# Optimization experiments

Measured on AMD Instinct MI355X. Metric: run time of the kernel, lower is better.

The kernel has to match this reference:

```python
import jax, jax.numpy as jnp
import numpy as np

EPS = 1e-3  # Keras BatchNormalization default epsilon


def _bn(x, gamma, beta, mean, var):
    # inference-mode batchnorm over channel axis 1 of [N,C,T,V]
    s = (gamma * jax.lax.rsqrt(var + EPS)).reshape(1, -1, 1, 1)
    b = (beta - gamma * mean * jax.lax.rsqrt(var + EPS)).reshape(1, -1, 1, 1)
    return x * s + b


def setup_inputs() -> dict:
    key = jax.random.key(0)
    ks = jax.random.split(key, 10)
    N, C, T, V, K, F, KT = 64, 64, 300, 25, 3, 64, 9
    x = jax.random.normal(ks[0], (N, C, T, V), jnp.float32)
    W1 = jax.random.normal(ks[1], (C, F * K), jnp.float32) * 0.05
    b1 = jnp.zeros((F * K,), jnp.float32)
    A = jax.random.normal(ks[2], (K, T, V, V), jnp.float32) * 0.2
    gamma1 = jnp.ones((F,), jnp.float32)
    beta1 = jnp.zeros((F,), jnp.float32)
    mean1 = jax.random.normal(ks[3], (F,), jnp.float32) * 0.1
    var1 = jax.random.uniform(ks[4], (F,), jnp.float32) + 0.5
    Wt = jax.random.normal(ks[5], (KT, 1, F, F), jnp.float32) * 0.05  # HWIO
    bt = jnp.zeros((F,), jnp.float32)
    gamma2 = jnp.ones((F,), jnp.float32)
    beta2 = jnp.zeros((F,), jnp.float32)
    mean2 = jax.random.normal(ks[6], (F,), jnp.float32) * 0.1
    var2 = jax.random.uniform(ks[7], (F,), jnp.float32) + 0.5
    return dict(x=x, W1=W1, b1=b1, A=A, gamma1=gamma1, beta1=beta1,
                mean1=mean1, var1=var1, Wt=Wt, bt=bt, gamma2=gamma2,
                beta2=beta2, mean2=mean2, var2=var2)


def reference(x, W1, b1, A, gamma1, beta1, mean1, var1, Wt, bt,
              gamma2, beta2, mean2, var2):
    N, C, T, V = x.shape
    K = A.shape[0]
    F = W1.shape[1] // K
    # SGTACN: 1x1 conv (channels_first) == channel matmul
    y = jnp.einsum('nctv,cf->nftv', x, W1) + b1.reshape(1, -1, 1, 1)
    y = y.reshape(N, K, F, T, V)
    # spatial graph contraction with learned per-timestep adjacency
    y = jnp.einsum('nkftv,ktvw->nftw', y, A)
    # tgcn: BN -> relu -> temporal conv [9,1] SAME -> BN
    y = jax.nn.relu(_bn(y, gamma1, beta1, mean1, var1))
    y = jax.lax.conv_general_dilated(
        y, Wt, window_strides=(1, 1), padding='SAME',
        dimension_numbers=('NCHW', 'HWIO', 'NCHW')) + bt.reshape(1, -1, 1, 1)
    y = _bn(y, gamma2, beta2, mean2, var2)
    # identity residual (stride=1, no downsample, C_in == filters) + relu
    return jax.nn.relu(y + x)
```

## Files before the change

kernel.cpp:

```cpp
#include <hip/hip_runtime.h>
#include <hip/hip_bf16.h>
#include <stdint.h>

#define EPS 1e-3f

typedef __attribute__((ext_vector_type(8))) short bf16x8;
typedef __attribute__((ext_vector_type(4))) float f32x4;

union B8U { bf16x8 v; uint32_t u[4]; };

__device__ inline uint32_t pk2(float a, float b) {
    __hip_bfloat162 p;
    p.x = __float2bfloat16(a);
    p.y = __float2bfloat16(b);
    return *(uint32_t*)&p;
}

__global__ __launch_bounds__(256) void k0_prep_small(
    const float* __restrict__ W1, const float* __restrict__ Wt,
    const float* __restrict__ A,
    uint16_t* __restrict__ W1t, uint16_t* __restrict__ Abf,
    float* __restrict__ csA_g)
{
    int i = blockIdx.x * 256 + threadIdx.x;
    if (i < 12288) {
        int f = i / 192, Kp = i % 192, k = Kp >> 6, c = Kp & 63;
        __hip_bfloat16 b = __float2bfloat16(W1[c * 192 + k * 64 + f]);
        W1t[i] = *(uint16_t*)&b;
    } else if (i < 49152) {
        int j = i - 12288;
        int jj = j & 7, fo = (j >> 3) & 63, kb = j >> 9;
        int kk = kb * 8 + jj, dt = kk >> 6, fi = kk & 63;
        __hip_bfloat16 b = __float2bfloat16(Wt[(dt * 64 + fi) * 64 + fo]);
        Abf[j] = *(uint16_t*)&b;
    } else if (i < 71652) {
        int j = i - 49152;
        int k = j / 7500, r = j % 7500;
        int t = r / 25, w = r % 25;
        float s = 0.f;
        for (int v = 0; v < 25; ++v)
            s += A[((k * 300 + t) * 25 + v) * 25 + w];
        csA_g[j] = s;
    }
}

__global__ __launch_bounds__(256) void k0_prep_At(
    const float* __restrict__ A, uint16_t* __restrict__ At_g)
{
    int i = blockIdx.x * 256 + threadIdx.x;
    if (i < 921600) {
        int v = i & 31, w = (i >> 5) & 31, rest = i >> 10;
        int t = rest % 300, k = rest / 300;
        float val = 0.f;
        if (v < 25 && w < 25)
            val = A[((k * 300 + t) * 25 + v) * 25 + w];
        __hip_bfloat16 b = __float2bfloat16(val);
        At_g[i] = *(uint16_t*)&b;
    }
}

#define K1_SMEM 80512
__global__ __launch_bounds__(256) void k1_fused(
    const float* __restrict__ x, const uint16_t* __restrict__ At_g,
    const uint16_t* __restrict__ W1t, const float* __restrict__ csA_g,
    const float* __restrict__ b1,
    const float* __restrict__ gamma1, const float* __restrict__ beta1,
    const float* __restrict__ mean1, const float* __restrict__ var1,
    uint32_t* __restrict__ h2u)
{
    extern __shared__ __align__(16) char smem[];
    float* csA_s = (float*)(smem + 76800);
    float* s1s   = (float*)(smem + 79200);
    float* b1ns  = (float*)(smem + 79456);
    float* b1s   = (float*)(smem + 79712);

    const int t0   = blockIdx.x * 8;
    const int n    = blockIdx.y;
    const int tid  = threadIdx.x;
    const int lane = tid & 63, wv = tid >> 6;
    const int l15  = lane & 15, g = lane >> 4;
    int vc = (300 - t0) * 25; if (vc > 200) vc = 200;
    const int validcols = vc;

    for (int i = tid; i < 600; i += 256) {
        int k = i / 200, cr = i % 200;
        csA_s[k * 200 + cr] = (cr < validcols) ? csA_g[k * 7500 + t0 * 25 + cr] : 0.f;
    }
    if (tid < 64) {
        float rs = rsqrtf(var1[tid] + EPS);
        s1s[tid]  = gamma1[tid] * rs;
        b1ns[tid] = beta1[tid] - gamma1[tid] * mean1[tid] * rs;
    }
    if (tid >= 64 && tid < 256) b1s[tid - 64] = b1[tid - 64];

    for (int ti = 0; ti < 2; ++ti) {
        const int trel = wv * 2 + ti;
        const int t = t0 + trel;
        if (t >= 300) continue;

        bf16x8 a[4];
        const float* xb = x + (size_t)n * 480000 + t * 25;
        #pragma unroll
        for (int mf = 0; mf < 4; ++mf) {
            const int c = l15 + mf * 16;
            const float* xr = xb + (size_t)c * 7500;
            B8U ua;
            if (g < 3) {
                #pragma unroll
                for (int p = 0; p < 4; ++p)
                    ua.u[p] = pk2(xr[g * 8 + 2 * p], xr[g * 8 + 2 * p + 1]);
            } else {
                ua.u[0] = pk2(xr[24], 0.f);
                ua.u[1] = 0; ua.u[2] = 0; ua.u[3] = 0;
            }
            a[mf] = ua.v;
        }

        f32x4 acc[4][6];
        #pragma unroll
        for (int mf = 0; mf < 4; ++mf)
            #pragma unroll
            for (int nf = 0; nf < 6; ++nf)
                acc[mf][nf] = (f32x4){0.f, 0.f, 0.f, 0.f};

        #pragma unroll
        for (int nf = 0; nf < 6; ++nf) {
            const int col = nf * 16 + l15;
            const int k = col >> 5, w = col & 31;
            bf16x8 b = *(const bf16x8*)(At_g + (((k * 300 + t) * 32 + w) * 32 + g * 8));
            acc[0][nf] = __builtin_amdgcn_mfma_f32_16x16x32_bf16(a[0], b, acc[0][nf], 0, 0, 0);
            acc[1][nf] = __builtin_amdgcn_mfma_f32_16x16x32_bf16(a[1], b, acc[1][nf], 0, 0, 0);
            acc[2][nf] = __builtin_amdgcn_mfma_f32_16x16x32_bf16(a[2], b, acc[2][nf], 0, 0, 0);
            acc[3][nf] = __builtin_amdgcn_mfma_f32_16x16x32_bf16(a[3], b, acc[3][nf], 0, 0, 0);
        }

        #pragma unroll
        for (int nf = 0; nf < 6; ++nf) {
            const int col = nf * 16 + l15;
            const int k = col >> 5, w = col & 31;
            if (w < 25) {
                const int colrow = trel * 25 + w;
                const int sw = (w & 7) << 4;
                #pragma unroll
                for (int mf = 0; mf < 4; ++mf) {
                    const int c0 = mf * 16 + g * 4;
                    const int off = colrow * 384 + (((k * 64 + c0) * 2) ^ sw);
                    uint2 val;
                    val.x = pk2(acc[mf][nf][0], acc[mf][nf][1]);
                    val.y = pk2(acc[mf][nf][2], acc[mf][nf][3]);
                    *(uint2*)(smem + off) = val;
                }
            }
        }
    }
    __syncthreads();

    const int nfbase = (wv == 0) ? 0 : 1 + 3 * wv;
    const int nfcnt  = (wv == 0) ? 4 : 3;

    int coladdr[4], swz[4], colv[4];
    #pragma unroll
    for (int q = 0; q < 4; ++q) {
        int col = (nfbase + q) * 16 + l15;
        colv[q] = col;
        coladdr[q] = col * 384;
        swz[q] = ((col % 25) & 7) << 4;
    }

    f32x4 accz[4][4];
    #pragma unroll
    for (int mf = 0; mf < 4; ++mf)
        #pragma unroll
        for (int q = 0; q < 4; ++q)
            accz[mf][q] = (f32x4){0.f, 0.f, 0.f, 0.f};

    for (int kb = 0; kb < 6; ++kb) {
        bf16x8 a[4];
        #pragma unroll
        for (int mf = 0; mf < 4; ++mf) {
            int f = l15 + mf * 16;
            a[mf] = *(const bf16x8*)(W1t + f * 192 + kb * 32 + g * 8);
        }
        #pragma unroll
        for (int q = 0; q < 4; ++q) {
            if (q < nfcnt) {
                bf16x8 b = *(const bf16x8*)(smem + coladdr[q] + ((kb * 64 + g * 16) ^ swz[q]));
                accz[0][q] = __builtin_amdgcn_mfma_f32_16x16x32_bf16(a[0], b, accz[0][q], 0, 0, 0);
                accz[1][q] = __builtin_amdgcn_mfma_f32_16x16x32_bf16(a[1], b, accz[1][q], 0, 0, 0);
                accz[2][q] = __builtin_amdgcn_mfma_f32_16x16x32_bf16(a[2], b, accz[2][q], 0, 0, 0);
                accz[3][q] = __builtin_amdgcn_mfma_f32_16x16x32_bf16(a[3], b, accz[3][q], 0, 0, 0);
            }
        }
    }

    const uint32_t hbase = (uint32_t)(n * 300 + t0) * 800;
    #pragma unroll
    for (int q = 0; q < 4; ++q) {
        if (q < nfcnt) {
            const int col = colv[q];
            if (col < validcols) {
                const int trel = col / 25, w = col - trel * 25;
                const float cs0 = csA_s[col];
                const float cs1 = csA_s[200 + col];
                const float cs2 = csA_s[400 + col];
                const uint32_t rowbase = hbase + trel * 800 + w * 32;
                #pragma unroll
                for (int mf = 0; mf < 4; ++mf) {
                    const int f0 = mf * 16 + g * 4;
                    float zz[4];
                    #pragma unroll
                    for (int r = 0; r < 4; ++r) {
                        const int f = f0 + r;
                        float z = accz[mf][q][r]
                                + b1s[f] * cs0 + b1s[64 + f] * cs1 + b1s[128 + f] * cs2;
                        z = z * s1s[f] + b1ns[f];
                        zz[r] = fmaxf(z, 0.f);
                    }
                    uint2 st;
                    st.x = pk2(zz[0], zz[1]);
                    st.y = pk2(zz[2], zz[3]);
                    *(uint2*)(h2u + rowbase + (f0 >> 1)) = st;
                }
            }
        }
    }
}

#define K2_SMEM 77312
__global__ __launch_bounds__(256) void k2_mfma(
    const char* __restrict__ h2b,
    const uint16_t* __restrict__ Abf,
    const float* __restrict__ bt,
    const float* __restrict__ gamma2, const float* __restrict__ beta2,
    const float* __restrict__ mean2,  const float* __restrict__ var2,
    const float* __restrict__ x,
    float* __restrict__ out)
{
    extern __shared__ __align__(16) char smem2[];
    char*  lds_h = smem2;
    float* s2s   = (float*)(smem2 + 76800);
    float* b2s   = s2s + 64;

    const int t0  = blockIdx.x * 16;
    const int n   = blockIdx.y;
    const int tid = threadIdx.x;

    if (tid < 64) {
        float rs = rsqrtf(var2[tid] + EPS);
        float s  = gamma2[tid] * rs;
        s2s[tid] = s;
        b2s[tid] = beta2[tid] - gamma2[tid] * mean2[tid] * rs + bt[tid] * s;
    }

    const size_t hn = (size_t)n * 300 * 3200;
    for (int c = tid; c < 4800; c += 256) {
        int rr = c >> 3, c8 = c & 7;
        int trow = rr / 25;
        int w = rr - trow * 25;
        int tg = t0 - 4 + trow;
        int4 v = make_int4(0, 0, 0, 0);
        if (tg >= 0 && tg < 300)
            v = *(const int4*)(h2b + hn + (size_t)tg * 3200 + w * 128 + (c8 << 4));
        int s = c << 4;
        *(int4*)(lds_h + (s ^ (((s >> 7) & 7) << 4))) = v;
    }
    __syncthreads();

    const int wv = tid >> 6, lane = tid & 63;
    const int l15 = lane & 15, g = lane >> 4;
    const int colbase = wv * 112;
    const int nfr = (wv == 3) ? 4 : 7;

    f32x4 acc[4][7];
    #pragma unroll
    for (int mf = 0; mf < 4; ++mf)
        #pragma unroll
        for (int nf = 0; nf < 7; ++nf)
            acc[mf][nf] = (f32x4){0.f, 0.f, 0.f, 0.f};

    for (int kk = 0; kk < 18; ++kk) {
        const int dt   = kk >> 1;
        const int half = (kk & 1) << 6;
        const int kb   = kk * 4 + g;
        bf16x8 a[4];
        #pragma unroll
        for (int mf = 0; mf < 4; ++mf)
            a[mf] = *(const bf16x8*)(Abf + (kb * 64 + l15 + mf * 16) * 8);
        #pragma unroll
        for (int nf = 0; nf < 7; ++nf) {
            if (nf < nfr) {
                int r = colbase + (nf << 4) + l15 + 25 * dt;
                int s = (r << 7) + half + (g << 4);
                bf16x8 b = *(const bf16x8*)(lds_h + (s ^ ((r & 7) << 4)));
                acc[0][nf] = __builtin_amdgcn_mfma_f32_16x16x32_bf16(a[0], b, acc[0][nf], 0, 0, 0);
                acc[1][nf] = __builtin_amdgcn_mfma_f32_16x16x32_bf16(a[1], b, acc[1][nf], 0, 0, 0);
                acc[2][nf] = __builtin_amdgcn_mfma_f32_16x16x32_bf16(a[2], b, acc[2][nf], 0, 0, 0);
                acc[3][nf] = __builtin_amdgcn_mfma_f32_16x16x32_bf16(a[3], b, acc[3][nf], 0, 0, 0);
            }
        }
    }

    const size_t outn = (size_t)n * 480000;
    #pragma unroll
    for (int mf = 0; mf < 4; ++mf) {
        #pragma unroll
        for (int nf = 0; nf < 7; ++nf) {
            if (nf < nfr) {
                int col  = colbase + (nf << 4) + l15;
                int gcol = t0 * 25 + col;
                if (gcol < 7500) {
                    #pragma unroll
                    for (int reg = 0; reg < 4; ++reg) {
                        int fo = (mf << 4) + (g << 2) + reg;
                        size_t ga = outn + (size_t)fo * 7500 + gcol;
                        float val = acc[mf][nf][reg] * s2s[fo] + b2s[fo];
                        out[ga] = fmaxf(val + x[ga], 0.f);
                    }
                }
            }
        }
    }
}

extern "C" void kernel_launch(void* const* d_in, const int* in_sizes, int n_in,
                              void* d_out, int out_size, void* d_ws, size_t ws_size,
                              hipStream_t stream) {
    const float* x      = (const float*)d_in[0];
    const float* W1     = (const float*)d_in[1];
    const float* b1     = (const float*)d_in[2];
    const float* A      = (const float*)d_in[3];
    const float* gamma1 = (const float*)d_in[4];
    const float* beta1  = (const float*)d_in[5];
    const float* mean1  = (const float*)d_in[6];
    const float* var1   = (const float*)d_in[7];
    const float* Wt     = (const float*)d_in[8];
    const float* bt     = (const float*)d_in[9];
    const float* gamma2 = (const float*)d_in[10];
    const float* beta2  = (const float*)d_in[11];
    const float* mean2  = (const float*)d_in[12];
    const float* var2   = (const float*)d_in[13];
    float* out = (float*)d_out;

    char* ws = (char*)d_ws;
    uint32_t* h2u   = (uint32_t*)ws;
    char*     h2b   = ws;
    uint16_t* At_g  = (uint16_t*)(ws + 61440000);
    uint16_t* W1t   = (uint16_t*)(ws + 63283200);
    uint16_t* Abf   = (uint16_t*)(ws + 63307776);
    float*    csA_g = (float*)   (ws + 63381504);

    hipFuncSetAttribute((const void*)k1_fused,
                        hipFuncAttributeMaxDynamicSharedMemorySize, K1_SMEM);
    hipFuncSetAttribute((const void*)k2_mfma,
                        hipFuncAttributeMaxDynamicSharedMemorySize, K2_SMEM);

    k0_prep_small<<<280, 256, 0, stream>>>(W1, Wt, A, W1t, Abf, csA_g);
    k0_prep_At<<<3600, 256, 0, stream>>>(A, At_g);
    k1_fused<<<dim3(38, 64), 256, K1_SMEM, stream>>>(
        x, At_g, W1t, csA_g, b1, gamma1, beta1, mean1, var1, h2u);
    k2_mfma<<<dim3(19, 64), 256, K2_SMEM, stream>>>(
        h2b, Abf, bt, gamma2, beta2, mean2, var2, x, out);
}
```

Before: 452.5 us.

## Stage x tile cooperatively in LDS and halve k1 time tile to four steps

k1 now processes 4 timesteps per block instead of 8, one per wave, doubling the grid and cutting LDS use so more blocks fit per CU. The x tile is loaded cooperatively by all threads with coalesced-ish reads, converted to bf16 and stored into swizzled LDS, then read back as MFMA fragments, replacing strided per-lane global gathers. Adjacency fragments are prefetched into registers before the staging. The tail handling disappears because 300 is divisible by 4, at the cost of an extra barrier and more redundant setup per block.

```diff
diff --git a/kernel.cpp b/kernel.cpp
--- a/kernel.cpp
+++ b/kernel.cpp
@@ -6,8 +6,6 @@
 
 typedef __attribute__((ext_vector_type(8))) short bf16x8;
 typedef __attribute__((ext_vector_type(4))) float f32x4;
-
-union B8U { bf16x8 v; uint32_t u[4]; };
 
 __device__ inline uint32_t pk2(float a, float b) {
     __hip_bfloat162 p;
@@ -59,7 +57,8 @@
     }
 }
 
-#define K1_SMEM 80512
+#define K1_SMEM 61872
+#define XBASE 43008
 __global__ __launch_bounds__(256) void k1_fused(
     const float* __restrict__ x, const uint16_t* __restrict__ At_g,
     const uint16_t* __restrict__ W1t, const float* __restrict__ csA_g,
@@ -69,22 +68,46 @@
     uint32_t* __restrict__ h2u)
 {
     extern __shared__ __align__(16) char smem[];
-    float* csA_s = (float*)(smem + 76800);
-    float* s1s   = (float*)(smem + 79200);
-    float* b1ns  = (float*)(smem + 79456);
-    float* b1s   = (float*)(smem + 79712);
-
-    const int t0   = blockIdx.x * 8;
+    float* csA_s = (float*)(smem + 59392);
+    float* s1s   = (float*)(smem + 60592);
+    float* b1ns  = (float*)(smem + 60848);
+    float* b1s   = (float*)(smem + 61104);
+
+    const int t0   = blockIdx.x * 4;
     const int n    = blockIdx.y;
     const int tid  = threadIdx.x;
     const int lane = tid & 63, wv = tid >> 6;
     const int l15  = lane & 15, g = lane >> 4;
-    int vc = (300 - t0) * 25; if (vc > 200) vc = 200;
-    const int validcols = vc;
-
-    for (int i = tid; i < 600; i += 256) {
-        int k = i / 200, cr = i % 200;
-        csA_s[k * 200 + cr] = (cr < validcols) ? csA_g[k * 7500 + t0 * 25 + cr] : 0.f;
+
+    const int tw = t0 + wv;
+    bf16x8 bfr[6];
+    #pragma unroll
+    for (int nf = 0; nf < 6; ++nf) {
+        const int col = nf * 16 + l15;
+        const int k = col >> 5, w = col & 31;
+        bfr[nf] = *(const bf16x8*)(At_g + (((k * 300 + tw) * 32 + w) * 32 + g * 8));
+    }
+
+    const float* xn = x + (size_t)n * 480000;
+    for (int it = tid; it < 3328; it += 256) {
+        const int c = it / 52;
+        const int r = it % 52;
+        const int trel = r / 13, vp = r % 13;
+        const int v = vp * 2;
+        const float* p = xn + c * 7500 + (t0 + trel) * 25 + v;
+        const int slot = XBASE + (((((v >> 3) * 64 + c) * 4 + trel) * 16) ^ ((c & 7) << 4));
+        if (vp < 12) {
+            *(uint32_t*)(smem + slot + ((v & 7) << 1)) = pk2(p[0], p[1]);
+        } else {
+            *(uint32_t*)(smem + slot + 0)  = pk2(p[0], 0.f);
+            *(uint32_t*)(smem + slot + 4)  = 0u;
+            *(uint32_t*)(smem + slot + 8)  = 0u;
+            *(uint32_t*)(smem + slot + 12) = 0u;
+        }
+    }
+    for (int i = tid; i < 300; i += 256) {
+        int k = i / 100, cr = i % 100;
+        csA_s[i] = csA_g[k * 7500 + t0 * 25 + cr];
     }
     if (tid < 64) {
         float rs = rsqrtf(var1[tid] + EPS);
@@ -92,129 +115,107 @@
         b1ns[tid] = beta1[tid] - gamma1[tid] * mean1[tid] * rs;
     }
     if (tid >= 64 && tid < 256) b1s[tid - 64] = b1[tid - 64];
-
-    for (int ti = 0; ti < 2; ++ti) {
-        const int trel = wv * 2 + ti;
-        const int t = t0 + trel;
-        if (t >= 300) continue;
-
-        bf16x8 a[4];
-        const float* xb = x + (size_t)n * 480000 + t * 25;
-        #pragma unroll
-        for (int mf = 0; mf < 4; ++mf) {
-            const int c = l15 + mf * 16;
-            const float* xr = xb + (size_t)c * 7500;
-            B8U ua;
-            if (g < 3) {
-                #pragma unroll
-                for (int p = 0; p < 4; ++p)
-                    ua.u[p] = pk2(xr[g * 8 + 2 * p], xr[g * 8 + 2 * p + 1]);
-            } else {
-                ua.u[0] = pk2(xr[24], 0.f);
-                ua.u[1] = 0; ua.u[2] = 0; ua.u[3] = 0;
-            }
-            a[mf] = ua.v;
-        }
-
-        f32x4 acc[4][6];
-        #pragma unroll
-        for (int mf = 0; mf < 4; ++mf)
+    __syncthreads();
+
+    bf16x8 a[4];
+    #pragma unroll
+    for (int mf = 0; mf < 4; ++mf) {
+        const int c = l15 + 16 * mf;
+        const int sb = XBASE + ((((g * 64 + c) * 4 + wv) * 16) ^ ((c & 7) << 4));
+        a[mf] = *(const bf16x8*)(smem + sb);
+    }
+
+    f32x4 acc[4][6];
+    #pragma unroll
+    for (int mf = 0; mf < 4; ++mf)
+        #pragma unroll
+        for (int nf = 0; nf < 6; ++nf)
+            acc[mf][nf] = (f32x4){0.f, 0.f, 0.f, 0.f};
+
+    #pragma unroll
+    for (int nf = 0; nf < 6; ++nf) {
+        acc[0][nf] = __builtin_amdgcn_mfma_f32_16x16x32_bf16(a[0], bfr[nf], acc[0][nf], 0, 0, 0);
+        acc[1][nf] = __builtin_amdgcn_mfma_f32_16x16x32_bf16(a[1], bfr[nf], acc[1][nf], 0, 0, 0);
+        acc[2][nf] = __builtin_amdgcn_mfma_f32_16x16x32_bf16(a[2], bfr[nf], acc[2][nf], 0, 0, 0);
+        acc[3][nf] = __builtin_amdgcn_mfma_f32_16x16x32_bf16(a[3], bfr[nf], acc[3][nf], 0, 0, 0);
+    }
+
+    #pragma unroll
+    for (int nf = 0; nf < 6; ++nf) {
+        const int col = nf * 16 + l15;
+        const int k = col >> 5, w = col & 31;
+        if (w < 25) {
+            const int colrow = wv * 25 + w;
+            const int sw = (w & 7) << 4;
             #pragma unroll
-            for (int nf = 0; nf < 6; ++nf)
-                acc[mf][nf] = (f32x4){0.f, 0.f, 0.f, 0.f};
-
-        #pragma unroll
-        for (int nf = 0; nf < 6; ++nf) {
-            const int col = nf * 16 + l15;
-            const int k = col >> 5, w = col & 31;
-            bf16x8 b = *(const bf16x8*)(At_g + (((k * 300 + t) * 32 + w) * 32 + g * 8));
-            acc[0][nf] = __builtin_amdgcn_mfma_f32_16x16x32_bf16(a[0], b, acc[0][nf], 0, 0, 0);
-            acc[1][nf] = __builtin_amdgcn_mfma_f32_16x16x32_bf16(a[1], b, acc[1][nf], 0, 0, 0);
-            acc[2][nf] = __builtin_amdgcn_mfma_f32_16x16x32_bf16(a[2], b, acc[2][nf], 0, 0, 0);
-            acc[3][nf] = __builtin_amdgcn_mfma_f32_16x16x32_bf16(a[3], b, acc[3][nf], 0, 0, 0);
-        }
-
-        #pragma unroll
-        for (int nf = 0; nf < 6; ++nf) {
-            const int col = nf * 16 + l15;
-            const int k = col >> 5, w = col & 31;
-            if (w < 25) {
-                const int colrow = trel * 25 + w;
-                const int sw = (w & 7) << 4;
-                #pragma unroll
-                for (int mf = 0; mf < 4; ++mf) {
-                    const int c0 = mf * 16 + g * 4;
-                    const int off = colrow * 384 + (((k * 64 + c0) * 2) ^ sw);
-                    uint2 val;
-                    val.x = pk2(acc[mf][nf][0], acc[mf][nf][1]);
-                    val.y = pk2(acc[mf][nf][2], acc[mf][nf][3]);
-                    *(uint2*)(smem + off) = val;
-                }
+            for (int mf = 0; mf < 4; ++mf) {
+                const int c0 = mf * 16 + g * 4;
+                const int off = colrow * 384 + (((k * 64 + c0) * 2) ^ sw);
+                uint2 val;
+                val.x = pk2(acc[mf][nf][0], acc[mf][nf][1]);
+                val.y = pk2(acc[mf][nf][2], acc[mf][nf][3]);
+                *(uint2*)(smem + off) = val;
             }
         }
     }
     __syncthreads();
 
-    const int nfbase = (wv == 0) ? 0 : 1 + 3 * wv;
-    const int nfcnt  = (wv == 0) ? 4 : 3;
-
-    int coladdr[4], swz[4], colv[4];
-    #pragma unroll
-    for (int q = 0; q < 4; ++q) {
-        int col = (nfbase + q) * 16 + l15;
+    int colv[2], coladdr[2], swz[2], nq = (wv < 3) ? 2 : 1;
+    #pragma unroll
+    for (int q = 0; q < 2; ++q) {
+        int fr = wv + 4 * q;
+        int col = fr * 16 + l15;
         colv[q] = col;
         coladdr[q] = col * 384;
         swz[q] = ((col % 25) & 7) << 4;
     }
 
-    f32x4 accz[4][4];
+    f32x4 accz[4][2];
     #pragma unroll
     for (int mf = 0; mf < 4; ++mf)
         #pragma unroll
-        for (int q = 0; q < 4; ++q)
+        for (int q = 0; q < 2; ++q)
             accz[mf][q] = (f32x4){0.f, 0.f, 0.f, 0.f};
 
     for (int kb = 0; kb < 6; ++kb) {
-        bf16x8 a[4];
-        #pragma unroll
-        for (int mf = 0; mf < 4; ++mf) {
-            int f = l15 + mf * 16;
-            a[mf] = *(const bf16x8*)(W1t + f * 192 + kb * 32 + g * 8);
-        }
-        #pragma unroll
-        for (int q = 0; q < 4; ++q) {
-            if (q < nfcnt) {
+        bf16x8 az[4];
+        #pragma unroll
+        for (int mf = 0; mf < 4; ++mf)
+            az[mf] = *(const bf16x8*)(W1t + (l15 + 16 * mf) * 192 + kb * 32 + g * 8);
+        #pragma unroll
+        for (int q = 0; q < 2; ++q) {
+            if (q < nq) {
                 bf16x8 b = *(const bf16x8*)(smem + coladdr[q] + ((kb * 64 + g * 16) ^ swz[q]));
-                accz[0][q] = __builtin_amdgcn_mfma_f32_16x16x32_bf16(a[0], b, accz[0][q], 0, 0, 0);
-                accz[1][q] = __builtin_amdgcn_mfma_f32_16x16x32_bf16(a[1], b, accz[1][q], 0, 0, 0);
-                accz[2][q] = __builtin_amdgcn_mfma_f32_16x16x32_bf16(a[2], b, accz[2][q], 0, 0, 0);
-                accz[3][q] = __builtin_amdgcn_mfma_f32_16x16x32_bf16(a[3], b, accz[3][q], 0, 0, 0);
+                accz[0][q] = __builtin_amdgcn_mfma_f32_16x16x32_bf16(az[0], b, accz[0][q], 0, 0, 0);
+                accz[1][q] = __builtin_amdgcn_mfma_f32_16x16x32_bf16(az[1], b, accz[1][q], 0, 0, 0);
+                accz[2][q] = __builtin_amdgcn_mfma_f32_16x16x32_bf16(az[2], b, accz[2][q], 0, 0, 0);
+                accz[3][q] = __builtin_amdgcn_mfma_f32_16x16x32_bf16(az[3], b, accz[3][q], 0, 0, 0);
             }
         }
     }
 
     const uint32_t hbase = (uint32_t)(n * 300 + t0) * 800;
     #pragma unroll
-    for (int q = 0; q < 4; ++q) {
-        if (q < nfcnt) {
+    for (int q = 0; q < 2; ++q) {
+        if (q < nq) {
             const int col = colv[q];
-            if (col < validcols) {
+            if (col < 100) {
                 const int trel = col / 25, w = col - trel * 25;
                 const float cs0 = csA_s[col];
-                const float cs1 = csA_s[200 + col];
-                const float cs2 = csA_s[400 + col];
+                const float cs1 = csA_s[100 + col];
+                const float cs2 = csA_s[200 + col];
                 const uint32_t rowbase = hbase + trel * 800 + w * 32;
                 #pragma unroll
                 for (int mf = 0; mf < 4; ++mf) {
                     const int f0 = mf * 16 + g * 4;
                     float zz[4];
                     #pragma unroll
-                    for (int r = 0; r < 4; ++r) {
-                        const int f = f0 + r;
-                        float z = accz[mf][q][r]
+                    for (int rg = 0; rg < 4; ++rg) {
+                        const int f = f0 + rg;
+                        float z = accz[mf][q][rg]
                                 + b1s[f] * cs0 + b1s[64 + f] * cs1 + b1s[128 + f] * cs2;
                         z = z * s1s[f] + b1ns[f];
-                        zz[r] = fmaxf(z, 0.f);
+                        zz[rg] = fmaxf(z, 0.f);
                     }
                     uint2 st;
                     st.x = pk2(zz[0], zz[1]);
@@ -356,7 +357,7 @@
 
     k0_prep_small<<<280, 256, 0, stream>>>(W1, Wt, A, W1t, Abf, csA_g);
     k0_prep_At<<<3600, 256, 0, stream>>>(A, At_g);
-    k1_fused<<<dim3(38, 64), 256, K1_SMEM, stream>>>(
+    k1_fused<<<dim3(75, 64), 256, K1_SMEM, stream>>>(
         x, At_g, W1t, csA_g, b1, gamma1, beta1, mean1, var1, h2u);
     k2_mfma<<<dim3(19, 64), 256, K2_SMEM, stream>>>(
         h2b, Abf, bt, gamma2, beta2, mean2, var2, x, out);
```

New measurement: 519.3 us. 1.15x slower.
